# Performance work log

Hardware: AMD Instinct MI355X
Metric: run time of the kernel (lower is better)

## Reference

```python
import jax, jax.numpy as jnp
import numpy as np

N = 20000      # nodes per type
E = 320000     # edges per relation
F = 512        # raw feature dim
H = 4          # attention heads
C = 128        # hidden_channels per head
B = 64         # batch_size (num graphs)
HH = H * C
INNER = 64
NEG_SLOPE = 0.2


def _gatv2(x_src, x_dst, ei, Wl, Wr, att, b):
    """PyG GATv2Conv (concat=True, add_self_loops=True, neg_slope=0.2).
    x_src:[Ns,Fin] x_dst:[Nd,Fin'] ei:[2,E] Wl,Wr:[Fin,H*C] att:[H,C] b:[H*C].
    Returns [Nd, H*C]. Self-loop edges appended (inputs assumed loop-free)."""
    n_dst = x_dst.shape[0]
    loop = jnp.arange(min(x_src.shape[0], n_dst), dtype=ei.dtype)
    src = jnp.concatenate([ei[0], loop])
    dst = jnp.concatenate([ei[1], loop])
    xl = (x_src @ Wl).reshape(-1, H, C)   # source-side transform
    xr = (x_dst @ Wr).reshape(-1, H, C)   # target-side transform
    e = jax.nn.leaky_relu(xl[src] + xr[dst], NEG_SLOPE)   # [E',H,C]
    logit = jnp.einsum('ehc,hc->eh', e, att)               # [E',H]
    m = jax.ops.segment_max(logit, dst, num_segments=n_dst)
    m = jnp.where(jnp.isfinite(m), m, 0.0)
    p = jnp.exp(logit - m[dst])
    s = jax.ops.segment_sum(p, dst, num_segments=n_dst)
    alpha = p / jnp.maximum(s[dst], 1e-16)                 # per-dst softmax
    out = jax.ops.segment_sum(alpha[:, :, None] * xl[src], dst, num_segments=n_dst)
    return out.reshape(n_dst, HH) + b


def _layer(x_i, x_j, ei_ii, ei_jj, ei_ij, ei_ji, Wl, Wr, att, b):
    # relation order: 0:(x_i->x_i) 1:(x_j->x_j) 2:(x_i->x_j) 3:(x_j->x_i); HeteroConv aggr='sum'
    oi = _gatv2(x_i, x_i, ei_ii, Wl[0], Wr[0], att[0], b[0]) \
       + _gatv2(x_j, x_i, ei_ji, Wl[3], Wr[3], att[3], b[3])
    oj = _gatv2(x_j, x_j, ei_jj, Wl[1], Wr[1], att[1], b[1]) \
       + _gatv2(x_i, x_j, ei_ij, Wl[2], Wr[2], att[2], b[2])
    # head-sum + tanh: x.view(-1, heads, hidden).sum(1).tanh()
    oi = jnp.tanh(oi.reshape(-1, H, C).sum(axis=1))
    oj = jnp.tanh(oj.reshape(-1, H, C).sum(axis=1))
    return oi, oj


def setup_inputs() -> dict:
    key = jax.random.key(0)
    ks = jax.random.split(key, 24)
    inp = {
        'x_i': jax.random.normal(ks[0], (N, F), jnp.float32),
        'x_j': jax.random.normal(ks[1], (N, F), jnp.float32),
        'ei_ii': jax.random.randint(ks[2], (2, E), 0, N, jnp.int32),
        'ei_jj': jax.random.randint(ks[3], (2, E), 0, N, jnp.int32),
        'ei_ij': jax.random.randint(ks[4], (2, E), 0, N, jnp.int32),
        'ei_ji': jax.random.randint(ks[5], (2, E), 0, N, jnp.int32),
        'batch_i': jnp.sort(jax.random.randint(ks[6], (N,), 0, B, jnp.int32)),
        'batch_j': jnp.sort(jax.random.randint(ks[7], (N,), 0, B, jnp.int32)),
        'Wl0': jax.random.normal(ks[8], (4, F, HH), jnp.float32) / np.sqrt(F),
        'Wr0': jax.random.normal(ks[9], (4, F, HH), jnp.float32) / np.sqrt(F),
        'att0': jax.random.normal(ks[10], (4, H, C), jnp.float32) / np.sqrt(C),
        'b0': jnp.zeros((4, HH), jnp.float32),
        'Wl1': jax.random.normal(ks[11], (4, C, HH), jnp.float32) / np.sqrt(C),
        'Wr1': jax.random.normal(ks[12], (4, C, HH), jnp.float32) / np.sqrt(C),
        'att1': jax.random.normal(ks[13], (4, H, C), jnp.float32) / np.sqrt(C),
        'b1': jnp.zeros((4, HH), jnp.float32),
        'W_out': jax.random.normal(ks[14], (C, 1), jnp.float32) / np.sqrt(C),
        'b_out': jnp.zeros((1,), jnp.float32),
        'W_i': jax.random.normal(ks[15], (C, INNER), jnp.float32) / np.sqrt(C),
        'b_i': jnp.zeros((INNER,), jnp.float32),
        'W_j': jax.random.normal(ks[16], (C, INNER), jnp.float32) / np.sqrt(C),
        'b_j': jnp.zeros((INNER,), jnp.float32),
    }
    return inp


def reference(x_i, x_j, ei_ii, ei_jj, ei_ij, ei_ji, batch_i, batch_j,
              Wl0, Wr0, att0, b0, Wl1, Wr1, att1, b1,
              W_out, b_out, W_i, b_i, W_j, b_j):
    x_i, x_j = _layer(x_i, x_j, ei_ii, ei_jj, ei_ij, ei_ji, Wl0, Wr0, att0, b0)
    x_i, x_j = _layer(x_i, x_j, ei_ii, ei_jj, ei_ij, ei_ji, Wl1, Wr1, att1, b1)
    # global_add_pool per graph, then unsqueeze(1) + tanh
    p_i = jnp.tanh(jax.ops.segment_sum(x_i, batch_i, num_segments=B))[:, None, :]  # [B,1,C]
    p_j = jnp.tanh(jax.ops.segment_sum(x_j, batch_j, num_segments=B))[:, None, :]
    y_i = p_i @ W_i + b_i   # [B,1,INNER]
    y_j = p_j @ W_j + b_j
    x = (p_i + p_j)[:, 0, :]            # cat along dim=1 then sum(dim=1)
    logits = jax.nn.sigmoid(x @ W_out + b_out)   # [B,1]
    return (logits, y_i, y_j)
```

## Files before the change

### kernel.cpp

```cpp
#include <hip/hip_runtime.h>

#define NN      20000
#define EE      320000
#define ETOT    340000
#define FD      512
#define HH_     4
#define CD      128
#define HHD     512
#define BG      64
#define INNERD  64

typedef __attribute__((ext_vector_type(8))) short bf16x8;
typedef __attribute__((ext_vector_type(4))) float f32x4;

__device__ __forceinline__ float bf2f(unsigned v) { return __uint_as_float(v << 16); }
__device__ __forceinline__ unsigned short f2bf(float f) {
    unsigned u = __float_as_uint(f);
    unsigned r = 0x7fffu + ((u >> 16) & 1u);
    return (unsigned short)((u + r) >> 16);
}
__device__ __forceinline__ void load8bf(const unsigned short* p, float* f) {
    uint4 u = *reinterpret_cast<const uint4*>(p);
    f[0] = bf2f(u.x & 0xffffu); f[1] = bf2f(u.x >> 16);
    f[2] = bf2f(u.y & 0xffffu); f[3] = bf2f(u.y >> 16);
    f[4] = bf2f(u.z & 0xffffu); f[5] = bf2f(u.z >> 16);
    f[6] = bf2f(u.w & 0xffffu); f[7] = bf2f(u.w >> 16);
}
__device__ __forceinline__ void split_f32(float x, unsigned short& hi, unsigned short& lo) {
    unsigned u = __float_as_uint(x);
    hi = (unsigned short)(u >> 16);
    float r = x - bf2f(hi);
    lo = (unsigned short)(__float_as_uint(r) >> 16);
}
template <typename TA>
__device__ __forceinline__ void splitA(const TA* p, size_t i, unsigned short& hi, unsigned short& lo);
template <>
__device__ __forceinline__ void splitA<float>(const float* p, size_t i, unsigned short& hi, unsigned short& lo) {
    split_f32(p[i], hi, lo);
}
template <>
__device__ __forceinline__ void splitA<unsigned short>(const unsigned short* p, size_t i, unsigned short& hi, unsigned short& lo) {
    hi = p[i]; lo = 0;
}

__global__ __launch_bounds__(256) void csr_hist(const int* __restrict__ ei, int* __restrict__ cnt) {
    int e = blockIdx.x * blockDim.x + threadIdx.x;
    if (e < EE) atomicAdd(&cnt[ei[EE + e]], 1);
}

__global__ __launch_bounds__(1024) void csr_scan(const int* __restrict__ cnt,
                                                 int* __restrict__ rowptr,
                                                 int* __restrict__ cursor) {
    __shared__ int part[1024];
    int t = threadIdx.x;
    int base = t * 20;
    int s = 0;
    #pragma unroll
    for (int i = 0; i < 20; ++i) { int n = base + i; if (n < NN) s += cnt[n] + 1; }
    part[t] = s;
    __syncthreads();
    for (int off = 1; off < 1024; off <<= 1) {
        int v = (t >= off) ? part[t - off] : 0;
        __syncthreads();
        part[t] += v;
        __syncthreads();
    }
    int run = (t > 0) ? part[t - 1] : 0;
    #pragma unroll
    for (int i = 0; i < 20; ++i) {
        int n = base + i;
        if (n < NN) { rowptr[n] = run; cursor[n] = run; run += cnt[n] + 1; }
    }
    if (t == 1023) rowptr[NN] = run;
}

__global__ __launch_bounds__(256) void csr_scatter16(const int* __restrict__ ei,
                                                     int* __restrict__ cursor,
                                                     unsigned short* __restrict__ srcs) {
    int idx = blockIdx.x * blockDim.x + threadIdx.x;
    if (idx >= ETOT) return;
    int src, dst;
    if (idx < EE) { src = ei[idx]; dst = ei[EE + idx]; }
    else          { src = dst = idx - EE; }
    int pos = atomicAdd(&cursor[dst], 1);
    srcs[pos] = (unsigned short)src;
}

__global__ __launch_bounds__(256) void wsplit_t(const float* __restrict__ W,
                                                unsigned short* __restrict__ Whi,
                                                unsigned short* __restrict__ Wlo,
                                                int K)
{
    __shared__ float tile[64][65];
    const int nt = 512 / 64;
    const int kt = K / 64;
    int bid = blockIdx.x;
    int in = bid % nt; int ik = (bid / nt) % kt; int r = bid / (nt * kt);
    int t = threadIdx.x;
    const float* Wr_ = W + (size_t)r * K * 512;
    #pragma unroll
    for (int rep = 0; rep < 16; ++rep) {
        int idx = rep * 256 + t;
        int kk = idx >> 6, nn = idx & 63;
        tile[kk][nn] = Wr_[(size_t)(ik * 64 + kk) * 512 + in * 64 + nn];
    }
    __syncthreads();
    #pragma unroll
    for (int rep = 0; rep < 16; ++rep) {
        int idx = rep * 256 + t;
        int nn = idx >> 6, kk = idx & 63;
        unsigned short h, l; split_f32(tile[kk][nn], h, l);
        size_t o = ((size_t)r * 512 + in * 64 + nn) * K + ik * 64 + kk;
        Whi[o] = h; Wlo[o] = l;
    }
}

template <typename TA, bool A_EXACT>
__device__ __forceinline__ void gemm_body(
    const TA* __restrict__ A, const unsigned short* __restrict__ Bhg,
    const unsigned short* __restrict__ Blg, unsigned short* __restrict__ C,
    int bx, int by, int M, int K, int N)
{
    __shared__ unsigned short Ah[128][40];
    __shared__ unsigned short Al[A_EXACT ? 1 : 128][40];
    __shared__ unsigned short Bh[128][40];
    __shared__ unsigned short Bl[128][40];

    const int tid = threadIdx.x;
    const int wave = tid >> 6, lane = tid & 63;
    const int quad = lane >> 4, lrow = lane & 15;
    const int wr = (wave >> 1) * 64, wc = (wave & 1) * 64;
    const int tileM = by * 128, tileN = bx * 128;

    const int srow = tid >> 1;
    const int sks  = (tid & 1) * 16;
    const int sgm  = tileM + srow;

    f32x4 acc[4][4] = {};

    for (int k0 = 0; k0 < K; k0 += 32) {
        if constexpr (!A_EXACT) {
            bf16x8 ph[2] = {{}, {}}, pl[2] = {{}, {}};
            if (sgm < M) {
                const float* Ap = (const float*)A + (size_t)sgm * K + k0 + sks;
                #pragma unroll
                for (int s = 0; s < 2; ++s) {
                    float4 f0 = reinterpret_cast<const float4*>(Ap)[2 * s];
                    float4 f1 = reinterpret_cast<const float4*>(Ap)[2 * s + 1];
                    float xv[8] = {f0.x, f0.y, f0.z, f0.w, f1.x, f1.y, f1.z, f1.w};
                    #pragma unroll
                    for (int pp = 0; pp < 4; ++pp) {
                        unsigned u0 = __float_as_uint(xv[2 * pp]);
                        unsigned u1 = __float_as_uint(xv[2 * pp + 1]);
                        reinterpret_cast<unsigned*>(&ph[s])[pp] =
                            __builtin_amdgcn_perm(u1, u0, 0x07060302u);
                        float r0 = xv[2 * pp]     - __uint_as_float(u0 & 0xffff0000u);
                        float r1 = xv[2 * pp + 1] - __uint_as_float(u1 & 0xffff0000u);
                        reinterpret_cast<unsigned*>(&pl[s])[pp] =
                            __builtin_amdgcn_perm(__float_as_uint(r1), __float_as_uint(r0), 0x07060302u);
                    }
                }
            }
            *reinterpret_cast<bf16x8*>(&Ah[srow][sks])     = ph[0];
            *reinterpret_cast<bf16x8*>(&Ah[srow][sks + 8]) = ph[1];
            *reinterpret_cast<bf16x8*>(&Al[srow][sks])     = pl[0];
            *reinterpret_cast<bf16x8*>(&Al[srow][sks + 8]) = pl[1];
        } else {
            bf16x8 v0 = {}, v1 = {};
            if (sgm < M) {
                const unsigned short* Ap = (const unsigned short*)A + (size_t)sgm * K + k0 + sks;
                v0 = reinterpret_cast<const bf16x8*>(Ap)[0];
                v1 = reinterpret_cast<const bf16x8*>(Ap)[1];
            }
            *reinterpret_cast<bf16x8*>(&Ah[srow][sks])     = v0;
            *reinterpret_cast<bf16x8*>(&Ah[srow][sks + 8]) = v1;
        }
        {
            const unsigned short* Bp = Bhg + (size_t)(tileN + srow) * K + k0 + sks;
            const unsigned short* Bq = Blg + (size_t)(tileN + srow) * K + k0 + sks;
            bf16x8 h0 = reinterpret_cast<const bf16x8*>(Bp)[0];
            bf16x8 h1 = reinterpret_cast<const bf16x8*>(Bp)[1];
            bf16x8 l0 = reinterpret_cast<const bf16x8*>(Bq)[0];
            bf16x8 l1 = reinterpret_cast<const bf16x8*>(Bq)[1];
            *reinterpret_cast<bf16x8*>(&Bh[srow][sks])     = h0;
            *reinterpret_cast<bf16x8*>(&Bh[srow][sks + 8]) = h1;
            *reinterpret_cast<bf16x8*>(&Bl[srow][sks])     = l0;
            *reinterpret_cast<bf16x8*>(&Bl[srow][sks + 8]) = l1;
        }
        __syncthreads();
        bf16x8 ah[4], al[4], bh[4], bl[4];
        #pragma unroll
        for (int mi = 0; mi < 4; ++mi) {
            ah[mi] = *reinterpret_cast<const bf16x8*>(&Ah[wr + mi * 16 + lrow][quad * 8]);
            if constexpr (!A_EXACT)
                al[mi] = *reinterpret_cast<const bf16x8*>(&Al[wr + mi * 16 + lrow][quad * 8]);
        }
        #pragma unroll
        for (int ni = 0; ni < 4; ++ni) {
            bh[ni] = *reinterpret_cast<const bf16x8*>(&Bh[wc + ni * 16 + lrow][quad * 8]);
            bl[ni] = *reinterpret_cast<const bf16x8*>(&Bl[wc + ni * 16 + lrow][quad * 8]);
        }
        #pragma unroll
        for (int mi = 0; mi < 4; ++mi)
            #pragma unroll
            for (int ni = 0; ni < 4; ++ni) {
                acc[mi][ni] = __builtin_amdgcn_mfma_f32_16x16x32_bf16(
                    ah[mi], bh[ni], acc[mi][ni], 0, 0, 0);
                acc[mi][ni] = __builtin_amdgcn_mfma_f32_16x16x32_bf16(
                    ah[mi], bl[ni], acc[mi][ni], 0, 0, 0);
                if constexpr (!A_EXACT)
                    acc[mi][ni] = __builtin_amdgcn_mfma_f32_16x16x32_bf16(
                        al[mi], bh[ni], acc[mi][ni], 0, 0, 0);
            }
        __syncthreads();
    }
    #pragma unroll
    for (int mi = 0; mi < 4; ++mi) {
        #pragma unroll
        for (int ni = 0; ni < 4; ++ni) {
            int gcol = tileN + wc + ni * 16 + lrow;
            #pragma unroll
            for (int r = 0; r < 4; ++r) {
                int grow = tileM + wr + mi * 16 + quad * 4 + r;
                if (grow < M)
                    C[(size_t)grow * N + gcol] = f2bf(acc[mi][ni][r]);
            }
        }
    }
}

template <typename TA, bool A_EXACT>
__global__ __launch_bounds__(256, 3) void gemm_mfma_t(
    const TA* __restrict__ A0, const TA* __restrict__ A1,
    const unsigned short* __restrict__ B0h, const unsigned short* __restrict__ B0l,
    const unsigned short* __restrict__ B1h, const unsigned short* __restrict__ B1l,
    unsigned short* __restrict__ C0, unsigned short* __restrict__ C1,
    int M, int K, int N)
{
    const int gx = gridDim.x, gy = gridDim.y;
    const int nwg = gx * gy * (int)gridDim.z;
    int b = ((int)blockIdx.z * gy + blockIdx.y) * gx + blockIdx.x;
    int xcd = b & 7, q8 = nwg >> 3, r8 = nwg & 7;
    int work = (xcd < r8 ? xcd * (q8 + 1) : r8 * (q8 + 1) + (xcd - r8) * q8) + (b >> 3);
    int bx = work % gx; int t2 = work / gx; int by = t2 % gy; int bz = t2 / gy;

    const TA* A = bz ? A1 : A0;
    const unsigned short* Bhg = bz ? B1h : B0h;
    const unsigned short* Blg = bz ? B1l : B0l;
    unsigned short* C = bz ? C1 : C0;
    gemm_body<TA, A_EXACT>(A, Bhg, Blg, C, bx, by, M, K, N);
}

template <typename TA, bool A_EXACT>
__global__ __launch_bounds__(256, 3) void gemm_mfma_t4(
    const TA* __restrict__ A0, const TA* __restrict__ A1,
    const TA* __restrict__ A2, const TA* __restrict__ A3,
    const unsigned short* __restrict__ B0h, const unsigned short* __restrict__ B0l,
    const unsigned short* __restrict__ B1h, const unsigned short* __restrict__ B1l,
    const unsigned short* __restrict__ B2h, const unsigned short* __restrict__ B2l,
    const unsigned short* __restrict__ B3h, const unsigned short* __restrict__ B3l,
    unsigned short* __restrict__ C0, unsigned short* __restrict__ C1,
    unsigned short* __restrict__ C2, unsigned short* __restrict__ C3,
    int M, int K, int N)
{
    const int gx = gridDim.x, gy = gridDim.y;
    const int nwg = gx * gy * (int)gridDim.z;
    int b = ((int)blockIdx.z * gy + blockIdx.y) * gx + blockIdx.x;
    int xcd = b & 7, q8 = nwg >> 3, r8 = nwg & 7;
    int work = (xcd < r8 ? xcd * (q8 + 1) : r8 * (q8 + 1) + (xcd - r8) * q8) + (b >> 3);
    int bx = work % gx; int t2 = work / gx; int by = t2 % gy; int bz = t2 / gy;

    const TA* A = bz == 0 ? A0 : bz == 1 ? A1 : bz == 2 ? A2 : A3;
    const unsigned short* Bhg = bz == 0 ? B0h : bz == 1 ? B1h : bz == 2 ? B2h : B3h;
    const unsigned short* Blg = bz == 0 ? B0l : bz == 1 ? B1l : bz == 2 ? B2l : B3l;
    unsigned short* C = bz == 0 ? C0 : bz == 1 ? C1 : bz == 2 ? C2 : C3;
    gemm_body<TA, A_EXACT>(A, Bhg, Blg, C, bx, by, M, K, N);
}

template <typename TA, bool A_EXACT>
__global__ __launch_bounds__(256) void gemm_mfma(
    const TA* __restrict__ A0, const TA* __restrict__ A1,
    const float* __restrict__ B0, const float* __restrict__ B1, int ldb,
    unsigned short* __restrict__ C0, unsigned short* __restrict__ C1,
    int M, int K, int N)
{
    const TA* A = blockIdx.z ? A1 : A0;
    const float* B = blockIdx.z ? B1 : B0;
    unsigned short* C = blockIdx.z ? C1 : C0;

    __shared__ unsigned short Ah[64][40];
    __shared__ unsigned short Al[64][40];
    __shared__ unsigned short Bh[64][40];
    __shared__ unsigned short Bl[64][40];
    const int tid = threadIdx.x;
    const int wave = tid >> 6, lane = tid & 63;
    const int quad = lane >> 4, lrow = lane & 15;
    const int tileM = blockIdx.y * 64, tileN = blockIdx.x * 64;
    const int wm = (wave >> 1) * 32, wn = (wave & 1) * 32;

    f32x4 acc[2][2] = {};

    const int am = tid >> 2;
    const int aks = (tid & 3) * 8;
    const int bn = tid & 63;
    const int bk0 = (tid >> 6) * 8;

    for (int k0 = 0; k0 < K; k0 += 32) {
        {
            int gm = tileM + am;
            bf16x8 ph = {}, pl = {};
            if (gm < M) {
                #pragma unroll
                for (int j = 0; j < 8; ++j) {
                    unsigned short h, l;
                    splitA(A, (size_t)gm * K + k0 + aks + j, h, l);
                    ph[j] = (short)h; pl[j] = (short)l;
                }
            }
            *reinterpret_cast<bf16x8*>(&Ah[am][aks]) = ph;
            if (!A_EXACT) *reinterpret_cast<bf16x8*>(&Al[am][aks]) = pl;
        }
        {
            bf16x8 ph, pl;
            #pragma unroll
            for (int j = 0; j < 8; ++j) {
                unsigned short h, l;
                split_f32(B[(size_t)(k0 + bk0 + j) * ldb + tileN + bn], h, l);
                ph[j] = (short)h; pl[j] = (short)l;
            }
            *reinterpret_cast<bf16x8*>(&Bh[bn][bk0]) = ph;
            *reinterpret_cast<bf16x8*>(&Bl[bn][bk0]) = pl;
        }
        __syncthreads();
        bf16x8 ah[2], al[2], bh[2], bl[2];
        #pragma unroll
        for (int mi = 0; mi < 2; ++mi) {
            ah[mi] = *reinterpret_cast<const bf16x8*>(&Ah[wm + mi * 16 + lrow][quad * 8]);
            if (!A_EXACT)
                al[mi] = *reinterpret_cast<const bf16x8*>(&Al[wm + mi * 16 + lrow][quad * 8]);
        }
        #pragma unroll
        for (int ni = 0; ni < 2; ++ni) {
            bh[ni] = *reinterpret_cast<const bf16x8*>(&Bh[wn + ni * 16 + lrow][quad * 8]);
            bl[ni] = *reinterpret_cast<const bf16x8*>(&Bl[wn + ni * 16 + lrow][quad * 8]);
        }
        #pragma unroll
        for (int mi = 0; mi < 2; ++mi)
            #pragma unroll
            for (int ni = 0; ni < 2; ++ni) {
                acc[mi][ni] = __builtin_amdgcn_mfma_f32_16x16x32_bf16(
                    ah[mi], bh[ni], acc[mi][ni], 0, 0, 0);
                acc[mi][ni] = __builtin_amdgcn_mfma_f32_16x16x32_bf16(
                    ah[mi], bl[ni], acc[mi][ni], 0, 0, 0);
                if (!A_EXACT)
                    acc[mi][ni] = __builtin_amdgcn_mfma_f32_16x16x32_bf16(
                        al[mi], bh[ni], acc[mi][ni], 0, 0, 0);
            }
        __syncthreads();
    }
    #pragma unroll
    for (int mi = 0; mi < 2; ++mi) {
        #pragma unroll
        for (int ni = 0; ni < 2; ++ni) {
            int gcol = tileN + wn + ni * 16 + lrow;
            #pragma unroll
            for (int r = 0; r < 4; ++r) {
                int grow = tileM + wm + mi * 16 + quad * 4 + r;
                if (grow < M)
                    C[(size_t)grow * N + gcol] = f2bf(acc[mi][ni][r]);
            }
        }
    }
}

__global__ __launch_bounds__(256) void fused_aggr1(
    const int* __restrict__ rowptr, const unsigned short* __restrict__ srcs,
    const unsigned short* __restrict__ xl, const unsigned short* __restrict__ xr,
    const float* __restrict__ att,
    float* __restrict__ acc, int add_in, int fin_mode,
    const float* __restrict__ bA, const float* __restrict__ bB,
    unsigned short* __restrict__ z,
    const int* __restrict__ batch, float* __restrict__ pool)
{
    int dst = (int)((blockIdx.x * (size_t)blockDim.x + threadIdx.x) >> 6);
    int lane = threadIdx.x & 63;
    if (dst >= NN) return;
    int beg = rowptr[dst], end = rowptr[dst + 1];

    unsigned ub = *reinterpret_cast<const unsigned*>(xr + (size_t)dst * CD + lane * 2);
    float br0 = bf2f(ub & 0xffffu), br1 = bf2f(ub >> 16);
    float ta0 = att[lane * 2], ta1 = att[lane * 2 + 1];

    float n0 = 0.f, n1 = 0.f, den = 0.f;
    for (int k = beg; k < end; ++k) {
        int src = srcs[k];
        unsigned ua = *reinterpret_cast<const unsigned*>(xl + (size_t)src * CD + lane * 2);
        float a0 = bf2f(ua & 0xffffu), a1 = bf2f(ua >> 16);
        float v0 = a0 + br0, v1 = a1 + br1;
        v0 = (v0 > 0.f) ? v0 : 0.2f * v0;
        v1 = (v1 > 0.f) ? v1 : 0.2f * v1;
        float d = v0 * ta0 + v1 * ta1;
        #pragma unroll
        for (int off = 1; off < 64; off <<= 1)
            d += __shfl_xor(d, off);
        float p = expf(d);
        n0 += p * a0; n1 += p * a1; den += p;
    }
    float o0 = n0 / den, o1 = n1 / den;
    size_t ai = (size_t)dst * CD + lane * 2;
    if (add_in) { o0 += acc[ai]; o1 += acc[ai + 1]; }
    if (fin_mode == 0) {
        acc[ai] = o0; acc[ai + 1] = o1;
    } else {
        int c0 = lane * 2;
        float bb0 = 0.f, bb1 = 0.f;
        #pragma unroll
        for (int h = 0; h < HH_; ++h) {
            bb0 += bA[h * CD + c0]     + bB[h * CD + c0];
            bb1 += bA[h * CD + c0 + 1] + bB[h * CD + c0 + 1];
        }
        o0 = tanhf(o0 + bb0);
        o1 = tanhf(o1 + bb1);
        if (fin_mode == 1) {
            z[ai] = f2bf(o0); z[ai + 1] = f2bf(o1);
        } else {
            int b = batch[dst];
            atomicAdd(&pool[(size_t)b * CD + c0],     o0);
            atomicAdd(&pool[(size_t)b * CD + c0 + 1], o1);
        }
    }
}

__device__ __forceinline__ void gat_rel(
    const int* __restrict__ rp, const unsigned short* __restrict__ sr,
    const unsigned short* __restrict__ xl, const unsigned short* __restrict__ xr,
    const float* __restrict__ att, int dst, int lane, float* o)
{
    int beg = rp[dst], end = rp[dst + 1];
    float br[8], ta[8];
    load8bf(xr + (size_t)dst * HHD + lane * 8, br);
    #pragma unroll
    for (int j = 0; j < 8; ++j) ta[j] = att[lane * 8 + j];

    float n[8] = {}; float den = 0.f;
    int k = beg;
    for (; k + 2 <= end; k += 2) {
        int s0 = sr[k], s1 = sr[k + 1];
        float a0[8], a1[8];
        load8bf(xl + (size_t)s0 * HHD + lane * 8, a0);
        load8bf(xl + (size_t)s1 * HHD + lane * 8, a1);
        float d0 = 0.f, d1 = 0.f;
        #pragma unroll
        for (int j = 0; j < 8; ++j) {
            float v0 = a0[j] + br[j];
            v0 = (v0 > 0.f) ? v0 : 0.2f * v0;
            d0 += v0 * ta[j];
            float v1 = a1[j] + br[j];
            v1 = (v1 > 0.f) ? v1 : 0.2f * v1;
            d1 += v1 * ta[j];
        }
        d0 += __shfl_xor(d0, 1);  d1 += __shfl_xor(d1, 1);
        d0 += __shfl_xor(d0, 2);  d1 += __shfl_xor(d1, 2);
        d0 += __shfl_xor(d0, 4);  d1 += __shfl_xor(d1, 4);
        d0 += __shfl_xor(d0, 8);  d1 += __shfl_xor(d1, 8);
        float p0 = expf(d0), p1 = expf(d1);
        den += p0;
        #pragma unroll
        for (int j = 0; j < 8; ++j) n[j] += p0 * a0[j];
        den += p1;
        #pragma unroll
        for (int j = 0; j < 8; ++j) n[j] += p1 * a1[j];
    }
    if (k < end) {
        int s0 = sr[k];
        float a0[8];
        load8bf(xl + (size_t)s0 * HHD + lane * 8, a0);
        float d0 = 0.f;
        #pragma unroll
        for (int j = 0; j < 8; ++j) {
            float v0 = a0[j] + br[j];
            v0 = (v0 > 0.f) ? v0 : 0.2f * v0;
            d0 += v0 * ta[j];
        }
        d0 += __shfl_xor(d0, 1);
        d0 += __shfl_xor(d0, 2);
        d0 += __shfl_xor(d0, 4);
        d0 += __shfl_xor(d0, 8);
        float p0 = expf(d0);
        den += p0;
        #pragma unroll
        for (int j = 0; j < 8; ++j) n[j] += p0 * a0[j];
    }
    float inv = 1.f / den;
    #pragma unroll
    for (int j = 0; j < 8; ++j) {
        o[j] = n[j] * inv;
        o[j] += __shfl_xor(o[j], 16);
        o[j] += __shfl_xor(o[j], 32);
    }
}

__global__ __launch_bounds__(256) void fused_aggr4(
    const int* __restrict__ rowptr, const unsigned short* __restrict__ srcs,
    const unsigned short* __restrict__ xl, const unsigned short* __restrict__ xr,
    const float* __restrict__ att,
    float* __restrict__ acc, int add_in, int fin_mode,
    const float* __restrict__ bA, const float* __restrict__ bB,
    unsigned short* __restrict__ z,
    const int* __restrict__ batch, float* __restrict__ pool)
{
    int dst = (int)((blockIdx.x * (size_t)blockDim.x + threadIdx.x) >> 6);
    int lane = threadIdx.x & 63;
    if (dst >= NN) return;

    float o[8];
    gat_rel(rowptr, srcs, xl, xr, att, dst, lane, o);

    if (lane < 16) {
        size_t ai = (size_t)dst * CD + lane * 8;
        if (add_in) {
            #pragma unroll
            for (int j = 0; j < 8; ++j) o[j] += acc[ai + j];
        }
        if (fin_mode == 0) {
            #pragma unroll
            for (int j = 0; j < 8; ++j) acc[ai + j] = o[j];
        } else {
            int c0 = lane * 8;
            #pragma unroll
            for (int j = 0; j < 8; ++j) {
                float bb = 0.f;
                #pragma unroll
                for (int h = 0; h < HH_; ++h)
                    bb += bA[h * CD + c0 + j] + bB[h * CD + c0 + j];
                o[j] = tanhf(o[j] + bb);
            }
            if (fin_mode == 1) {
                #pragma unroll
                for (int j = 0; j < 8; ++j) z[ai + j] = f2bf(o[j]);
            } else {
                #pragma unroll
                for (int j = 0; j < 8; ++j) acc[ai + j] = o[j];
            }
        }
    }
}

__global__ __launch_bounds__(256) void fused_aggr4d(
    const int* __restrict__ rp0, const unsigned short* __restrict__ sr0,
    const unsigned short* __restrict__ xl0, const unsigned short* __restrict__ xr0,
    const float* __restrict__ attA,
    const int* __restrict__ rp1, const unsigned short* __restrict__ sr1,
    const unsigned short* __restrict__ xl1, const unsigned short* __restrict__ xr1,
    const float* __restrict__ attB,
    float* __restrict__ acc, int fin_mode,
    const float* __restrict__ bA, const float* __restrict__ bB,
    unsigned short* __restrict__ z,
    const int* __restrict__ batch, float* __restrict__ pool)
{
    int dst = (int)((blockIdx.x * (size_t)blockDim.x + threadIdx.x) >> 6);
    int lane = threadIdx.x & 63;
    if (dst >= NN) return;

    float o0[8], o1[8];
    gat_rel(rp0, sr0, xl0, xr0, attA, dst, lane, o0);
    gat_rel(rp1, sr1, xl1, xr1, attB, dst, lane, o1);
    #pragma unroll
    for (int j = 0; j < 8; ++j) o1[j] += o0[j];

    if (lane < 16) {
        size_t ai = (size_t)dst * CD + lane * 8;
        int c0 = lane * 8;
        #pragma unroll
        for (int j = 0; j < 8; ++j) {
            float bb = 0.f;
            #pragma unroll
            for (int h = 0; h < HH_; ++h)
                bb += bA[h * CD + c0 + j] + bB[h * CD + c0 + j];
            o1[j] = tanhf(o1[j] + bb);
        }
        if (fin_mode == 1) {
            #pragma unroll
            for (int j = 0; j < 8; ++j) z[ai + j] = f2bf(o1[j]);
        } else {
            #pragma unroll
            for (int j = 0; j < 8; ++j) acc[ai + j] = o1[j];
        }
    }
}

__global__ __launch_bounds__(512) void pool_reduce(
    const float* __restrict__ acc, const int* __restrict__ batch,
    float* __restrict__ pool)
{
    int b = blockIdx.x;
    int t = threadIdx.x & (CD - 1);
    int q = threadIdx.x >> 7;
    int lo, hi;
    { int l = 0, r = NN; while (l < r) { int m = (l + r) >> 1; if (batch[m] < b) l = m + 1; else r = m; } lo = l; }
    { int l = lo, r = NN; while (l < r) { int m = (l + r) >> 1; if (batch[m] <= b) l = m + 1; else r = m; } hi = l; }
    float s = 0.f;
    for (int nrow = lo + q; nrow < hi; nrow += 4)
        s += acc[(size_t)nrow * CD + t];
    __shared__ float red[4][CD];
    red[q][t] = s;
    __syncthreads();
    if (q == 0)
        pool[(size_t)b * CD + t] = red[0][t] + red[1][t] + red[2][t] + red[3][t];
}

__global__ __launch_bounds__(128) void head_kernel(
    const float* __restrict__ pool_i, const float* __restrict__ pool_j,
    const float* __restrict__ W_out, const float* __restrict__ b_out,
    const float* __restrict__ W_i, const float* __restrict__ b_i,
    const float* __restrict__ W_j, const float* __restrict__ b_j,
    float* __restrict__ out)
{
    int b = blockIdx.x;
    int t = threadIdx.x;
    __shared__ float pi[CD], pj[CD];
    pi[t] = tanhf(pool_i[(size_t)b * CD + t]);
    pj[t] = tanhf(pool_j[(size_t)b * CD + t]);
    __syncthreads();
    if (t < INNERD) {
        float a = b_i[t];
        for (int c = 0; c < CD; ++c) a += pi[c] * W_i[c * INNERD + t];
        out[BG + (size_t)b * INNERD + t] = a;
    } else {
        int k = t - INNERD;
        float a = b_j[k];
        for (int c = 0; c < CD; ++c) a += pj[c] * W_j[c * INNERD + k];
        out[BG + BG * INNERD + (size_t)b * INNERD + k] = a;
    }
    if (t == 0) {
        float a = b_out[0];
        for (int c = 0; c < CD; ++c) a += (pi[c] + pj[c]) * W_out[c];
        out[b] = 1.f / (1.f + expf(-a));
    }
}

struct Ws {
    unsigned short *xl, *xr, *xl2, *xr2, *z_i, *z_j;
    float* acc;
    int *rowptr[4];
    unsigned short *srcs[4];
    int *cnt, *cursor;
    float *pool_i, *pool_j;
    unsigned short *wt0l_h, *wt0l_l, *wt0r_h, *wt0r_l;
    unsigned short *wt1l_h, *wt1l_l, *wt1r_h, *wt1r_l;
};

static void build_csr(const int* ei, int* rowptr, unsigned short* srcs,
                      int* cnt, int* cursor, hipStream_t stream) {
    hipMemsetAsync(cnt, 0, NN * sizeof(int), stream);
    csr_hist<<<(EE + 255) / 256, 256, 0, stream>>>(ei, cnt);
    csr_scan<<<1, 1024, 0, stream>>>(cnt, rowptr, cursor);
    csr_scatter16<<<(ETOT + 255) / 256, 256, 0, stream>>>(ei, cursor, srcs);
}

template <typename TA, bool A_EXACT>
static void run_group_fat_m(const TA* srcA[2], const TA* dstA[2],
                            const int* rp[2], const unsigned short* sr[2],
                            const int rids[2], int K,
                            const unsigned short* WTl_h, const unsigned short* WTl_l,
                            const unsigned short* WTr_h, const unsigned short* WTr_l,
                            const float* att, const float* bias, int fin_mode,
                            unsigned short* zout, const int* batch, float* pool,
                            const Ws& w, hipStream_t stream)
{
    dim3 gg(HHD / 128, (NN + 127) / 128, 4);
    size_t off0 = (size_t)rids[0] * HHD * K;
    size_t off1 = (size_t)rids[1] * HHD * K;
    gemm_mfma_t4<TA, A_EXACT><<<gg, 256, 0, stream>>>(
        srcA[0], dstA[0], srcA[1], dstA[1],
        WTl_h + off0, WTl_l + off0, WTr_h + off0, WTr_l + off0,
        WTl_h + off1, WTl_l + off1, WTr_h + off1, WTr_l + off1,
        w.xl, w.xr, w.xl2, w.xr2, NN, K, HHD);
    fused_aggr4d<<<NN / 4, 256, 0, stream>>>(
        rp[0], sr[0], w.xl, w.xr, att + (size_t)rids[0] * HHD,
        rp[1], sr[1], w.xl2, w.xr2, att + (size_t)rids[1] * HHD,
        w.acc, fin_mode,
        bias + (size_t)rids[0] * HHD, bias + (size_t)rids[1] * HHD,
        zout, batch, pool);
}

template <typename TA, bool A_EXACT>
static void run_group_fat_t(const TA* srcA[2], const TA* dstA[2],
                            const int* rp[2], const unsigned short* sr[2],
                            const int rids[2], int K,
                            const unsigned short* WTl_h, const unsigned short* WTl_l,
                            const unsigned short* WTr_h, const unsigned short* WTr_l,
                            const float* att, const float* bias, int fin_mode,
                            unsigned short* zout, const int* batch, float* pool,
                            const Ws& w, hipStream_t stream)
{
    dim3 gg(HHD / 128, (NN + 127) / 128, 2);
    const int ablocks = NN / 4;
    for (int q = 0; q < 2; ++q) {
        int r = rids[q];
        size_t off = (size_t)r * HHD * K;
        gemm_mfma_t<TA, A_EXACT><<<gg, 256, 0, stream>>>(
            srcA[q], dstA[q],
            WTl_h + off, WTl_l + off, WTr_h + off, WTr_l + off,
            w.xl, w.xr, NN, K, HHD);
        int fm = (q == 1) ? fin_mode : 0;
        fused_aggr4<<<ablocks, 256, 0, stream>>>(
            rp[q], sr[q], w.xl, w.xr,
            att + (size_t)r * HHD,
            w.acc, q > 0 ? 1 : 0, fm,
            bias + (size_t)rids[0] * HHD, bias + (size_t)rids[1] * HHD,
            zout, batch, pool);
    }
}

template <typename TA, bool A_EXACT>
static void run_group_fat(const TA* srcA[2], const TA* dstA[2],
                          const int* rp[2], const unsigned short* sr[2],
                          const int rids[2], int K,
                          const float* Wl, const float* Wr, const float* att,
                          const float* bias, int fin_mode,
                          unsigned short* zout, const int* batch, float* pool,
                          const Ws& w, hipStream_t stream)
{
    dim3 gg(HHD / 64, (NN + 63) / 64, 2);
    const int ablocks = NN / 4;
    for (int q = 0; q < 2; ++q) {
        int r = rids[q];
        gemm_mfma<TA, A_EXACT><<<gg, 256, 0, stream>>>(
            srcA[q], dstA[q],
            Wl + (size_t)r * K * HHD, Wr + (size_t)r * K * HHD, HHD,
            w.xl, w.xr, NN, K, HHD);
        int fm = (q == 1) ? fin_mode : 0;
        fused_aggr4<<<ablocks, 256, 0, stream>>>(
            rp[q], sr[q], w.xl, w.xr,
            att + (size_t)r * HHD,
            w.acc, q > 0 ? 1 : 0, fm,
            bias + (size_t)rids[0] * HHD, bias + (size_t)rids[1] * HHD,
            zout, batch, pool);
    }
}

template <typename TA, bool A_EXACT>
static void run_group_thin(const TA* srcA[2], const TA* dstA[2],
                           const int* eis[2], const int rids[2], int K,
                           const float* Wl, const float* Wr, const float* att,
                           const float* bias, int fin_mode,
                           unsigned short* zout, const int* batch, float* pool,
                           const Ws& w, hipStream_t stream)
{
    dim3 gg(2, (NN + 63) / 64, 2);
    const int ablocks = NN / 4;
    for (int q = 0; q < 2; ++q) {
        int r = rids[q];
        build_csr(eis[q], w.rowptr[0], w.srcs[0], w.cnt, w.cursor, stream);
        for (int h = 0; h < HH_; ++h) {
            const float* WlS = Wl + (size_t)r * K * HHD + h * CD;
            const float* WrS = Wr + (size_t)r * K * HHD + h * CD;
            gemm_mfma<TA, A_EXACT><<<gg, 256, 0, stream>>>(
                srcA[q], dstA[q], WlS, WrS, HHD, w.xl, w.xr, NN, K, CD);
            int pass = q * HH_ + h;
            int fm = (pass == 2 * HH_ - 1) ? fin_mode : 0;
            fused_aggr1<<<ablocks, 256, 0, stream>>>(
                w.rowptr[0], w.srcs[0], w.xl, w.xr,
                att + (size_t)r * HHD + h * CD,
                w.acc, pass > 0 ? 1 : 0, fm,
                bias + (size_t)rids[0] * HHD, bias + (size_t)rids[1] * HHD,
                zout, batch, pool);
        }
    }
}

extern "C" void kernel_launch(void* const* d_in, const int* in_sizes, int n_in,
                              void* d_out, int out_size, void* d_ws, size_t ws_size,
                              hipStream_t stream)
{
    const float* x_i   = (const float*)d_in[0];
    const float* x_j   = (const float*)d_in[1];
    const int* ei_ii   = (const int*)d_in[2];
    const int* ei_jj   = (const int*)d_in[3];
    const int* ei_ij   = (const int*)d_in[4];
    const int* ei_ji   = (const int*)d_in[5];
    const int* batch_i = (const int*)d_in[6];
    const int* batch_j = (const int*)d_in[7];
    const float* Wl0   = (const float*)d_in[8];
    const float* Wr0   = (const float*)d_in[9];
    const float* att0  = (const float*)d_in[10];
    const float* b0    = (const float*)d_in[11];
    const float* Wl1   = (const float*)d_in[12];
    const float* Wr1   = (const float*)d_in[13];
    const float* att1  = (const float*)d_in[14];
    const float* b1    = (const float*)d_in[15];
    const float* W_out = (const float*)d_in[16];
    const float* b_out = (const float*)d_in[17];
    const float* W_i   = (const float*)d_in[18];
    const float* b_i   = (const float*)d_in[19];
    const float* W_j   = (const float*)d_in[20];
    const float* b_j   = (const float*)d_in[21];
    float* out = (float*)d_out;

    const size_t FAT2_BYTES = (size_t)NN * HHD * 2 * 2 + (size_t)NN * CD * 4
                            + (size_t)NN * CD * 2 * 2 + 4 * (size_t)ETOT * 2
                            + 4 * (size_t)(NN + 4) * 4 + (size_t)NN * 4 * 2
                            + (size_t)BG * CD * 4 * 2;
    const size_t FAT1_BYTES = (size_t)NN * HHD * 2 * 2 + (size_t)NN * CD * 4
                            + (size_t)NN * CD * 2 * 2 + (size_t)ETOT * 2
                            + (size_t)(NN + 4) * 4 + (size_t)NN * 4 * 2
                            + (size_t)BG * CD * 4 * 2;
    const size_t WT0_ONE = (size_t)4 * 512 * 512 * 2;
    const size_t WT1_ONE = (size_t)4 * 512 * 128 * 2;
    const size_t WT_BYTES = 4 * WT0_ONE + 4 * WT1_ONE;
    const size_t X2_BYTES = 2 * (size_t)NN * HHD * 2;

    const int ncsr = (ws_size >= FAT2_BYTES) ? 4 : 1;
    const bool fat = (ws_size >= FAT1_BYTES);
    const bool fat_t = (ws_size >= FAT2_BYTES + WT_BYTES);
    const bool fat_m = (ws_size >= FAT2_BYTES + WT_BYTES + X2_BYTES);

    Ws w;
    char* p = (char*)d_ws;
    size_t xbytes = fat ? (size_t)NN * HHD * 2 : (size_t)NN * CD * 2;
    w.xl     = (unsigned short*)p; p += xbytes;
    w.xr     = (unsigned short*)p; p += xbytes;
    w.acc    = (float*)p;          p += (size_t)NN * CD * 4;
    w.z_i    = (unsigned short*)p; p += (size_t)NN * CD * 2;
    w.z_j    = (unsigned short*)p; p += (size_t)NN * CD * 2;
    for (int r = 0; r < 4; ++r) {
        int rr = (r < ncsr) ? r : 0;
        if (r < ncsr) {
            w.rowptr[r] = (int*)p;            p += (size_t)(NN + 4) * 4;
            w.srcs[r]   = (unsigned short*)p; p += (size_t)ETOT * 2;
        } else {
            w.rowptr[r] = w.rowptr[rr]; w.srcs[r] = w.srcs[rr];
        }
    }
    w.cnt    = (int*)p;            p += (size_t)NN * 4;
    w.cursor = (int*)p;            p += (size_t)NN * 4;
    w.pool_i = (float*)p;          p += (size_t)BG * CD * 4;
    w.pool_j = (float*)p;          p += (size_t)BG * CD * 4;
    if (fat_t) {
        w.wt0l_h = (unsigned short*)p; p += WT0_ONE;
        w.wt0l_l = (unsigned short*)p; p += WT0_ONE;
        w.wt0r_h = (unsigned short*)p; p += WT0_ONE;
        w.wt0r_l = (unsigned short*)p; p += WT0_ONE;
        w.wt1l_h = (unsigned short*)p; p += WT1_ONE;
        w.wt1l_l = (unsigned short*)p; p += WT1_ONE;
        w.wt1r_h = (unsigned short*)p; p += WT1_ONE;
        w.wt1r_l = (unsigned short*)p; p += WT1_ONE;
    }
    if (fat_m) {
        w.xl2 = (unsigned short*)p; p += (size_t)NN * HHD * 2;
        w.xr2 = (unsigned short*)p; p += (size_t)NN * HHD * 2;
    }

    hipMemsetAsync(w.pool_i, 0, (size_t)BG * CD * sizeof(float), stream);
    hipMemsetAsync(w.pool_j, 0, (size_t)BG * CD * sizeof(float), stream);

    const int* eis_all[4] = { ei_ii, ei_jj, ei_ij, ei_ji };
    const float* srcA0_i[2] = { x_i, x_j };  const float* dstA0_i[2] = { x_i, x_i };
    const float* srcA0_j[2] = { x_j, x_i };  const float* dstA0_j[2] = { x_j, x_j };
    const int rids_i[2] = { 0, 3 };
    const int rids_j[2] = { 1, 2 };
    const unsigned short* srcA1_i[2] = { w.z_i, w.z_j };
    const unsigned short* dstA1_i[2] = { w.z_i, w.z_i };
    const unsigned short* srcA1_j[2] = { w.z_j, w.z_i };
    const unsigned short* dstA1_j[2] = { w.z_j, w.z_j };

    if (fat_t) {
        for (int r = 0; r < 4; ++r)
            build_csr(eis_all[r], w.rowptr[r], w.srcs[r], w.cnt, w.cursor, stream);
        wsplit_t<<<4 * (FD / 64) * 8, 256, 0, stream>>>(Wl0, w.wt0l_h, w.wt0l_l, FD);
        wsplit_t<<<4 * (FD / 64) * 8, 256, 0, stream>>>(Wr0, w.wt0r_h, w.wt0r_l, FD);
        wsplit_t<<<4 * (CD / 64) * 8, 256, 0, stream>>>(Wl1, w.wt1l_h, w.wt1l_l, CD);
        wsplit_t<<<4 * (CD / 64) * 8, 256, 0, stream>>>(Wr1, w.wt1r_h, w.wt1r_l, CD);

        const int* rp_i[2] = { w.rowptr[0], w.rowptr[3] };
        const unsigned short* sr_i[2] = { w.srcs[0], w.srcs[3] };
        const int* rp_j[2] = { w.rowptr[1], w.rowptr[2] };
        const unsigned short* sr_j[2] = { w.srcs[1], w.srcs[2] };

        if (fat_m) {
            run_group_fat_m<float, false>(srcA0_i, dstA0_i, rp_i, sr_i, rids_i, FD,
                                          w.wt0l_h, w.wt0l_l, w.wt0r_h, w.wt0r_l,
                                          att0, b0, 1, w.z_i, nullptr, nullptr, w, stream);
            run_group_fat_m<float, false>(srcA0_j, dstA0_j, rp_j, sr_j, rids_j, FD,
                                          w.wt0l_h, w.wt0l_l, w.wt0r_h, w.wt0r_l,
                                          att0, b0, 1, w.z_j, nullptr, nullptr, w, stream);
            run_group_fat_m<unsigned short, true>(srcA1_i, dstA1_i, rp_i, sr_i, rids_i, CD,
                                                  w.wt1l_h, w.wt1l_l, w.wt1r_h, w.wt1r_l,
                                                  att1, b1, 2, nullptr, batch_i, w.pool_i, w, stream);
            pool_reduce<<<BG, 512, 0, stream>>>(w.acc, batch_i, w.pool_i);
            run_group_fat_m<unsigned short, true>(srcA1_j, dstA1_j, rp_j, sr_j, rids_j, CD,
                                                  w.wt1l_h, w.wt1l_l, w.wt1r_h, w.wt1r_l,
                                                  att1, b1, 2, nullptr, batch_j, w.pool_j, w, stream);
            pool_reduce<<<BG, 512, 0, stream>>>(w.acc, batch_j, w.pool_j);
        } else {
            run_group_fat_t<float, false>(srcA0_i, dstA0_i, rp_i, sr_i, rids_i, FD,
                                          w.wt0l_h, w.wt0l_l, w.wt0r_h, w.wt0r_l,
                                          att0, b0, 1, w.z_i, nullptr, nullptr, w, stream);
            run_group_fat_t<float, false>(srcA0_j, dstA0_j, rp_j, sr_j, rids_j, FD,
                                          w.wt0l_h, w.wt0l_l, w.wt0r_h, w.wt0r_l,
                                          att0, b0, 1, w.z_j, nullptr, nullptr, w, stream);
            run_group_fat_t<unsigned short, true>(srcA1_i, dstA1_i, rp_i, sr_i, rids_i, CD,
                                                  w.wt1l_h, w.wt1l_l, w.wt1r_h, w.wt1r_l,
                                                  att1, b1, 2, nullptr, batch_i, w.pool_i, w, stream);
            pool_reduce<<<BG, 512, 0, stream>>>(w.acc, batch_i, w.pool_i);
            run_group_fat_t<unsigned short, true>(srcA1_j, dstA1_j, rp_j, sr_j, rids_j, CD,
                                                  w.wt1l_h, w.wt1l_l, w.wt1r_h, w.wt1r_l,
                                                  att1, b1, 2, nullptr, batch_j, w.pool_j, w, stream);
            pool_reduce<<<BG, 512, 0, stream>>>(w.acc, batch_j, w.pool_j);
        }
    } else if (fat) {
        if (ncsr == 4) {
            for (int r = 0; r < 4; ++r)
                build_csr(eis_all[r], w.rowptr[r], w.srcs[r], w.cnt, w.cursor, stream);
            const int* rp_i[2] = { w.rowptr[0], w.rowptr[3] };
            const unsigned short* sr_i[2] = { w.srcs[0], w.srcs[3] };
            const int* rp_j[2] = { w.rowptr[1], w.rowptr[2] };
            const unsigned short* sr_j[2] = { w.srcs[1], w.srcs[2] };
            run_group_fat<float, false>(srcA0_i, dstA0_i, rp_i, sr_i, rids_i, FD,
                                        Wl0, Wr0, att0, b0, 1, w.z_i, nullptr, nullptr, w, stream);
            run_group_fat<float, false>(srcA0_j, dstA0_j, rp_j, sr_j, rids_j, FD,
                                        Wl0, Wr0, att0, b0, 1, w.z_j, nullptr, nullptr, w, stream);
            run_group_fat<unsigned short, true>(srcA1_i, dstA1_i, rp_i, sr_i, rids_i, CD,
                                                Wl1, Wr1, att1, b1, 2, nullptr, batch_i, w.pool_i, w, stream);
            pool_reduce<<<BG, 512, 0, stream>>>(w.acc, batch_i, w.pool_i);
            run_group_fat<unsigned short, true>(srcA1_j, dstA1_j, rp_j, sr_j, rids_j, CD,
                                                Wl1, Wr1, att1, b1, 2, nullptr, batch_j, w.pool_j, w, stream);
            pool_reduce<<<BG, 512, 0, stream>>>(w.acc, batch_j, w.pool_j);
        } else {
            for (int pass = 0; pass < 4; ++pass) {
                const int* rids = (pass & 1) ? rids_j : rids_i;
                for (int q = 0; q < 2; ++q) {
                    int r = rids[q];
                    build_csr(eis_all[r], w.rowptr[0], w.srcs[0], w.cnt, w.cursor, stream);
                    dim3 gg(HHD / 64, (NN + 63) / 64, 2);
                    if (pass < 2) {
                        const float* sa = (pass == 0) ? srcA0_i[q] : srcA0_j[q];
                        const float* da = (pass == 0) ? dstA0_i[q] : dstA0_j[q];
                        gemm_mfma<float, false><<<gg, 256, 0, stream>>>(
                            sa, da, Wl0 + (size_t)r * FD * HHD, Wr0 + (size_t)r * FD * HHD,
                            HHD, w.xl, w.xr, NN, FD, HHD);
                        fused_aggr4<<<NN / 4, 256, 0, stream>>>(
                            w.rowptr[0], w.srcs[0], w.xl, w.xr, att0 + (size_t)r * HHD,
                            w.acc, q, (q == 1) ? 1 : 0,
                            b0 + (size_t)rids[0] * HHD, b0 + (size_t)rids[1] * HHD,
                            (pass == 0) ? w.z_i : w.z_j, nullptr, nullptr);
                    } else {
                        const unsigned short* sa = (pass == 2) ? srcA1_i[q] : srcA1_j[q];
                        const unsigned short* da = (pass == 2) ? dstA1_i[q] : dstA1_j[q];
                        gemm_mfma<unsigned short, true><<<gg, 256, 0, stream>>>(
                            sa, da, Wl1 + (size_t)r * CD * HHD, Wr1 + (size_t)r * CD * HHD,
                            HHD, w.xl, w.xr, NN, CD, HHD);
                        fused_aggr4<<<NN / 4, 256, 0, stream>>>(
                            w.rowptr[0], w.srcs[0], w.xl, w.xr, att1 + (size_t)r * HHD,
                            w.acc, q, (q == 1) ? 2 : 0,
                            b1 + (size_t)rids[0] * HHD, b1 + (size_t)rids[1] * HHD,
                            nullptr, (pass == 2) ? batch_i : batch_j,
                            (pass == 2) ? w.pool_i : w.pool_j);
                    }
                }
                if (pass == 2)
                    pool_reduce<<<BG, 512, 0, stream>>>(w.acc, batch_i, w.pool_i);
                else if (pass == 3)
                    pool_reduce<<<BG, 512, 0, stream>>>(w.acc, batch_j, w.pool_j);
            }
        }
    } else {
        const int* eis_i[2] = { ei_ii, ei_ji };
        const int* eis_j[2] = { ei_jj, ei_ij };
        run_group_thin<float, false>(srcA0_i, dstA0_i, eis_i, rids_i, FD, Wl0, Wr0, att0, b0,
                                     1, w.z_i, nullptr, nullptr, w, stream);
        run_group_thin<float, false>(srcA0_j, dstA0_j, eis_j, rids_j, FD, Wl0, Wr0, att0, b0,
                                     1, w.z_j, nullptr, nullptr, w, stream);
        run_group_thin<unsigned short, true>(srcA1_i, dstA1_i, eis_i, rids_i, CD, Wl1, Wr1, att1, b1,
                                             2, nullptr, batch_i, w.pool_i, w, stream);
        run_group_thin<unsigned short, true>(srcA1_j, dstA1_j, eis_j, rids_j, CD, Wl1, Wr1, att1, b1,
                                             2, nullptr, batch_j, w.pool_j, w, stream);
    }

    head_kernel<<<BG, 128, 0, stream>>>(w.pool_i, w.pool_j, W_out, b_out,
                                        W_i, b_i, W_j, b_j, out);
}
```

Before: 1.441 ms.

## Pre-swizzle weight fragments for direct global B loads; use fast exp and fmax leaky-relu

The weight split kernel now writes W hi/lo in a k-blocked layout of 32-wide chunks per output column. The GEMM can then load B fragments directly from global memory into registers instead of staging them through shared memory, which removes the B LDS tiles and their LDS traffic. The attention aggregation also swaps expf for __expf and computes leaky-relu as fmaxf(v, 0.2v). The trade-offs are that B tiles are re-fetched per wave rather than shared through LDS, and __expf gives slightly lower accuracy.

```diff
diff --git a/kernel.cpp b/kernel.cpp
--- a/kernel.cpp
+++ b/kernel.cpp
@@ -110,7 +110,9 @@
         int idx = rep * 256 + t;
         int nn = idx >> 6, kk = idx & 63;
         unsigned short h, l; split_f32(tile[kk][nn], h, l);
-        size_t o = ((size_t)r * 512 + in * 64 + nn) * K + ik * 64 + kk;
+        int n = in * 64 + nn;
+        int k = ik * 64 + kk;
+        size_t o = (size_t)r * 512 * K + ((size_t)(k >> 5) * 512 + n) * 32 + (k & 31);
         Whi[o] = h; Wlo[o] = l;
     }
 }
@@ -123,8 +125,6 @@
 {
     __shared__ unsigned short Ah[128][40];
     __shared__ unsigned short Al[A_EXACT ? 1 : 128][40];
-    __shared__ unsigned short Bh[128][40];
-    __shared__ unsigned short Bl[128][40];
 
     const int tid = threadIdx.x;
     const int wave = tid >> 6, lane = tid & 63;
@@ -135,6 +135,9 @@
     const int srow = tid >> 1;
     const int sks  = (tid & 1) * 16;
     const int sgm  = tileM + srow;
+
+    const size_t bfrag = ((size_t)(tileN + wc + lrow) << 5) + quad * 8;
+    const size_t kblk  = (size_t)N << 5;
 
     f32x4 acc[4][4] = {};
 
@@ -175,30 +178,23 @@
             *reinterpret_cast<bf16x8*>(&Ah[srow][sks])     = v0;
             *reinterpret_cast<bf16x8*>(&Ah[srow][sks + 8]) = v1;
         }
+        bf16x8 bh[4], bl[4];
         {
-            const unsigned short* Bp = Bhg + (size_t)(tileN + srow) * K + k0 + sks;
-            const unsigned short* Bq = Blg + (size_t)(tileN + srow) * K + k0 + sks;
-            bf16x8 h0 = reinterpret_cast<const bf16x8*>(Bp)[0];
-            bf16x8 h1 = reinterpret_cast<const bf16x8*>(Bp)[1];
-            bf16x8 l0 = reinterpret_cast<const bf16x8*>(Bq)[0];
-            bf16x8 l1 = reinterpret_cast<const bf16x8*>(Bq)[1];
-            *reinterpret_cast<bf16x8*>(&Bh[srow][sks])     = h0;
-            *reinterpret_cast<bf16x8*>(&Bh[srow][sks + 8]) = h1;
-            *reinterpret_cast<bf16x8*>(&Bl[srow][sks])     = l0;
-            *reinterpret_cast<bf16x8*>(&Bl[srow][sks + 8]) = l1;
+            const unsigned short* Bb = Bhg + (size_t)(k0 >> 5) * kblk + bfrag;
+            const unsigned short* Bc = Blg + (size_t)(k0 >> 5) * kblk + bfrag;
+            #pragma unroll
+            for (int ni = 0; ni < 4; ++ni) {
+                bh[ni] = *reinterpret_cast<const bf16x8*>(Bb + ((size_t)ni << 9));
+                bl[ni] = *reinterpret_cast<const bf16x8*>(Bc + ((size_t)ni << 9));
+            }
         }
         __syncthreads();
-        bf16x8 ah[4], al[4], bh[4], bl[4];
+        bf16x8 ah[4], al[4];
         #pragma unroll
         for (int mi = 0; mi < 4; ++mi) {
             ah[mi] = *reinterpret_cast<const bf16x8*>(&Ah[wr + mi * 16 + lrow][quad * 8]);
             if constexpr (!A_EXACT)
                 al[mi] = *reinterpret_cast<const bf16x8*>(&Al[wr + mi * 16 + lrow][quad * 8]);
-        }
-        #pragma unroll
-        for (int ni = 0; ni < 4; ++ni) {
-            bh[ni] = *reinterpret_cast<const bf16x8*>(&Bh[wc + ni * 16 + lrow][quad * 8]);
-            bl[ni] = *reinterpret_cast<const bf16x8*>(&Bl[wc + ni * 16 + lrow][quad * 8]);
         }
         #pragma unroll
         for (int mi = 0; mi < 4; ++mi)
@@ -453,17 +449,17 @@
         #pragma unroll
         for (int j = 0; j < 8; ++j) {
             float v0 = a0[j] + br[j];
-            v0 = (v0 > 0.f) ? v0 : 0.2f * v0;
+            v0 = fmaxf(v0, 0.2f * v0);
             d0 += v0 * ta[j];
             float v1 = a1[j] + br[j];
-            v1 = (v1 > 0.f) ? v1 : 0.2f * v1;
+            v1 = fmaxf(v1, 0.2f * v1);
             d1 += v1 * ta[j];
         }
         d0 += __shfl_xor(d0, 1);  d1 += __shfl_xor(d1, 1);
         d0 += __shfl_xor(d0, 2);  d1 += __shfl_xor(d1, 2);
         d0 += __shfl_xor(d0, 4);  d1 += __shfl_xor(d1, 4);
         d0 += __shfl_xor(d0, 8);  d1 += __shfl_xor(d1, 8);
-        float p0 = expf(d0), p1 = expf(d1);
+        float p0 = __expf(d0), p1 = __expf(d1);
         den += p0;
         #pragma unroll
         for (int j = 0; j < 8; ++j) n[j] += p0 * a0[j];
@@ -479,14 +475,14 @@
         #pragma unroll
         for (int j = 0; j < 8; ++j) {
             float v0 = a0[j] + br[j];
-            v0 = (v0 > 0.f) ? v0 : 0.2f * v0;
+            v0 = fmaxf(v0, 0.2f * v0);
             d0 += v0 * ta[j];
         }
         d0 += __shfl_xor(d0, 1);
         d0 += __shfl_xor(d0, 2);
         d0 += __shfl_xor(d0, 4);
         d0 += __shfl_xor(d0, 8);
-        float p0 = expf(d0);
+        float p0 = __expf(d0);
         den += p0;
         #pragma unroll
         for (int j = 0; j < 8; ++j) n[j] += p0 * a0[j];
```

Result: no change. 1.414 ms (-1.9%).
